# Kernel tuning notes

Hardware: AMD Instinct MI355X
Metric: run time of the kernel (lower is better)

Reference implementation:

```python
import jax, jax.numpy as jnp
import numpy as np

MODEL_DIM = 4096
HEAD_DIM = 128
N_HEADS = 32
N_KV_HEADS = 8
B = 2
S = 2048
ROPE_BASE = 10000.0


def _rope(v, pos):
    """Interleaved-pair rotary embedding (Llama style). v: [b, s, h, d]."""
    d = v.shape[-1]
    half = d // 2
    inv_freq = 1.0 / (ROPE_BASE ** (jnp.arange(half, dtype=jnp.float32) * 2.0 / d))
    t = pos + jnp.arange(v.shape[1], dtype=jnp.float32)          # [s]
    ang = t[:, None] * inv_freq                                   # [s, half]
    cos = jnp.cos(ang)[None, :, None, :].astype(v.dtype)          # [1, s, 1, half]
    sin = jnp.sin(ang)[None, :, None, :].astype(v.dtype)
    x1 = v[..., 0::2]
    x2 = v[..., 1::2]
    o1 = x1 * cos - x2 * sin
    o2 = x1 * sin + x2 * cos
    return jnp.stack([o1, o2], axis=-1).reshape(v.shape)


def setup_inputs() -> dict:
    key = jax.random.key(0)
    kx, kq, kk, kv, ko = jax.random.split(key, 5)
    wscale = MODEL_DIM ** -0.5  # keep pre-softmax logits in a sane range
    x = jax.random.normal(kx, (B, S, MODEL_DIM), dtype=jnp.float32)
    wq = jax.random.normal(kq, (HEAD_DIM * N_HEADS, MODEL_DIM), dtype=jnp.float32) * wscale
    wk = jax.random.normal(kk, (HEAD_DIM * N_KV_HEADS, MODEL_DIM), dtype=jnp.float32) * wscale
    wv = jax.random.normal(kv, (HEAD_DIM * N_KV_HEADS, MODEL_DIM), dtype=jnp.float32) * wscale
    wo = jax.random.normal(ko, (HEAD_DIM * N_HEADS, MODEL_DIM), dtype=jnp.float32).T * wscale
    wo = jnp.asarray(wo)  # [MODEL_DIM, HEAD_DIM*N_HEADS] like nn.Linear weight
    # causal additive mask, as SDPA attn_mask (float): 0 on/below diag, -inf above
    causal = jnp.tril(jnp.ones((S, S), dtype=bool))
    mask = jnp.where(causal, 0.0, -jnp.inf).astype(jnp.float32)
    return {"x": x, "wq": wq, "wk": wk, "wv": wv, "wo": wo, "mask": mask, "pos": 0}


def reference(x, wq, wk, wv, wo, mask, pos):
    b, s, _ = x.shape
    rep = N_HEADS // N_KV_HEADS
    q = (x @ wq.T).reshape(b, s, N_HEADS, HEAD_DIM)
    k = (x @ wk.T).reshape(b, s, N_KV_HEADS, HEAD_DIM)
    v = (x @ wv.T).reshape(b, s, N_KV_HEADS, HEAD_DIM)
    q = _rope(q, pos)
    k = _rope(k, pos)
    # With pos=0 prefill, the kv-cache slice [:, :pos+s] equals k, v just written.
    # GQA without materializing repeat_interleave: group q heads by kv head.
    qg = q.reshape(b, s, N_KV_HEADS, rep, HEAD_DIM)
    scale = HEAD_DIM ** -0.5
    scores = jnp.einsum('bqhrd,bkhd->bhrqk', qg, k) * scale        # [b, kvh, rep, s, s]
    scores = scores + mask                                          # broadcast [s, s]
    p = jax.nn.softmax(scores, axis=-1)
    out = jnp.einsum('bhrqk,bkhd->bqhrd', p, v).reshape(b, s, N_HEADS * HEAD_DIM)
    return out @ wo.T
```

## Files before the change

### kernel.cpp

```cpp
#include <hip/hip_runtime.h>
#include <hip/hip_bf16.h>
#include <stdint.h>

#define MODEL_DIM 4096
#define HEAD_DIM  128
#define NH        32
#define NKV       8
#define BB        2
#define SS        2048
#define ROWS      (BB*SS)
#define QKVN      (MODEL_DIM + 2*NKV*HEAD_DIM)
#define KOFF      MODEL_DIM
#define VOFF      (MODEL_DIM + NKV*HEAD_DIM)
#define SCALE_QK  0.08838834764831845f

typedef __attribute__((ext_vector_type(8))) short short8;
typedef __attribute__((ext_vector_type(4))) float f32x4;

static __device__ __forceinline__ unsigned short f2bf(float f) {
  union { float f; unsigned u; } v; v.f = f;
  unsigned r = v.u + 0x7fffu + ((v.u >> 16) & 1u);
  return (unsigned short)(r >> 16);
}
static __device__ __forceinline__ float bf2f(unsigned short u) {
  union { unsigned u; float f; } v; v.u = ((unsigned)u) << 16;
  return v.f;
}

__global__ void cvt_bf16(const float* __restrict__ s, unsigned short* __restrict__ d, int n4) {
  int i = blockIdx.x * blockDim.x + threadIdx.x;
  int st = gridDim.x * blockDim.x;
  for (; i < n4; i += st) {
    float4 v = reinterpret_cast<const float4*>(s)[i];
    ushort4 o;
    o.x = f2bf(v.x); o.y = f2bf(v.y); o.z = f2bf(v.z); o.w = f2bf(v.w);
    reinterpret_cast<ushort4*>(d)[i] = o;
  }
}

template<int OUT_F32>
__global__ __launch_bounds__(256) void gemm_bt(
    const unsigned short* __restrict__ A, const unsigned short* __restrict__ B,
    void* __restrict__ Cv, int M, int N, int K)
{
  __shared__ unsigned short As[128 * 32];
  __shared__ unsigned short Bs[128 * 32];
  const int tid  = threadIdx.x;
  const int lane = tid & 63;
  const int w    = tid >> 6;

  const int nwg = gridDim.x;
  const int bid = blockIdx.x;
  const int q8  = nwg >> 3;
  const int wg  = (bid & 7) * q8 + (bid >> 3);
  const int gm  = M >> 7;
  const int bm  = wg % gm, bn = wg / gm;
  const int m0  = bm << 7, n0 = bn << 7;
  const int wm  = (w >> 1) << 6, wn = (w & 1) << 6;

  f32x4 acc[4][4] = {};

  const int rowA = lane >> 2;
  const int ch8  = (lane & 3) * 8;

  for (int k0 = 0; k0 < K; k0 += 32) {
    __syncthreads();
    #pragma unroll
    for (int i = 0; i < 2; ++i) {
      const unsigned short* ga = A + (size_t)(m0 + i*64 + w*16 + rowA) * K + k0 + ch8;
      __builtin_amdgcn_global_load_lds((const __attribute__((address_space(1))) void*)ga,
          (__attribute__((address_space(3))) void*)&As[(i*64 + w*16) * 32], 16, 0, 0);
      const unsigned short* gb = B + (size_t)(n0 + i*64 + w*16 + rowA) * K + k0 + ch8;
      __builtin_amdgcn_global_load_lds((const __attribute__((address_space(1))) void*)gb,
          (__attribute__((address_space(3))) void*)&Bs[(i*64 + w*16) * 32], 16, 0, 0);
    }
    __syncthreads();

    short8 af[4], bf[4];
    const int fr = lane & 15, fg = lane >> 4;
    #pragma unroll
    for (int r = 0; r < 4; ++r)
      af[r] = *(const short8*)&As[(wm + r*16 + fr) * 32 + fg * 8];
    #pragma unroll
    for (int r = 0; r < 4; ++r)
      bf[r] = *(const short8*)&Bs[(wn + r*16 + fr) * 32 + fg * 8];
    #pragma unroll
    for (int i = 0; i < 4; ++i)
      #pragma unroll
      for (int j = 0; j < 4; ++j)
        acc[i][j] = __builtin_amdgcn_mfma_f32_16x16x32_bf16(af[i], bf[j], acc[i][j], 0, 0, 0);
  }

  const int cr = (lane >> 4) * 4, cc = lane & 15;
  #pragma unroll
  for (int i = 0; i < 4; ++i)
    #pragma unroll
    for (int j = 0; j < 4; ++j) {
      const int gr = m0 + wm + i*16 + cr;
      const int gc = n0 + wn + j*16 + cc;
      #pragma unroll
      for (int e = 0; e < 4; ++e) {
        const float v = acc[i][j][e];
        if (OUT_F32) ((float*)Cv)[(size_t)(gr + e) * N + gc] = v;
        else ((unsigned short*)Cv)[(size_t)(gr + e) * N + gc] = f2bf(v);
      }
    }
}

__global__ void rope_kernel(unsigned short* __restrict__ qkv, const int* __restrict__ posp) {
  const int row = blockIdx.x;
  const float t = (float)((row & (SS - 1)) + posp[0]);
  const float c0 = -13.28771237954945f / 64.0f;
  for (int i = threadIdx.x; i < (NH + NKV) * 64; i += blockDim.x) {
    const int hh = i >> 6, p = i & 63;
    const int colbase = (hh < NH) ? hh * HEAD_DIM : KOFF + (hh - NH) * HEAD_DIM;
    const float inv = exp2f((float)p * c0);
    float sn, cs;
    sincosf(t * inv, &sn, &cs);
    const size_t base = (size_t)row * QKVN + colbase + 2 * p;
    const float x1 = bf2f(qkv[base]), x2 = bf2f(qkv[base + 1]);
    qkv[base]     = f2bf(x1 * cs - x2 * sn);
    qkv[base + 1] = f2bf(x1 * sn + x2 * cs);
  }
}

#define QBLK 64
#define KVB  64
#define LDK  136
#define LDP  72

static __device__ __forceinline__ int vt_off(int d, int kv) {
  const int byte = (kv << 1) ^ ((((d & 7) ^ ((d >> 3) & 7))) << 4);
  return (d << 6) + (byte >> 1);
}

static __device__ __forceinline__ float bcast_row16(float v0, float v1, float v2, float v3, int lane) {
  const int sel = (lane >> 2) & 3;
  const float a = (sel & 1) ? v1 : v0;
  const float b = (sel & 1) ? v3 : v2;
  const float m = (sel & 2) ? b : a;
  const int q = lane & 15;
  return __shfl(m, ((q >> 2) << 4) + ((q & 3) << 2));
}

__global__ __launch_bounds__(256) void attn_kernel(
    const unsigned short* __restrict__ qkv, unsigned short* __restrict__ out)
{
  __shared__ unsigned short Ks[KVB * LDK];
  __shared__ unsigned short Vt[HEAD_DIM * KVB];
  __shared__ unsigned short Ps[4 * 16 * LDP];

  const int tid  = threadIdx.x;
  const int lane = tid & 63;
  const int w    = tid >> 6;
  const int bh   = blockIdx.y;
  const int b    = bh >> 5, h = bh & 31;
  const int kvh  = h >> 2;
  const int q0   = (gridDim.x - 1 - blockIdx.x) * QBLK;
  const int fr   = lane & 15, fg = lane >> 4;

  const size_t qrow0 = (size_t)(b * SS + q0 + w * 16);
  short8 qf[4];
  #pragma unroll
  for (int kk = 0; kk < 4; ++kk)
    qf[kk] = *(const short8*)&qkv[(qrow0 + fr) * QKVN + h * HEAD_DIM + kk * 32 + fg * 8];

  f32x4 ot[8] = {};
  float m_run[4], l_run[4];
  #pragma unroll
  for (int i = 0; i < 4; ++i) { m_run[i] = -INFINITY; l_run[i] = 0.f; }

  const int ntile = (q0 >> 6) + 1;
  for (int jt = 0; jt < ntile; ++jt) {
    const int j0 = jt * KVB;
    const bool diag = (jt == ntile - 1);
    __syncthreads();
    #pragma unroll
    for (int it = 0; it < 4; ++it) {
      const int cid = it * 256 + tid;
      const int row = cid >> 4, c8 = (cid & 15) << 3;
      const size_t grow = (size_t)(b * SS + j0 + row);
      *(uint4*)&Ks[row * LDK + c8] = *(const uint4*)&qkv[grow * QKVN + KOFF + kvh * HEAD_DIM + c8];
      uint4 vv = *(const uint4*)&qkv[grow * QKVN + VOFF + kvh * HEAD_DIM + c8];
      const unsigned short* v8 = (const unsigned short*)&vv;
      #pragma unroll
      for (int e = 0; e < 8; ++e)
        Vt[vt_off(c8 + e, row)] = v8[e];
    }
    __syncthreads();

    float pv[4][4];
    #pragma unroll
    for (int ct = 0; ct < 4; ++ct) {
      f32x4 s = {};
      #pragma unroll
      for (int kk = 0; kk < 4; ++kk) {
        const short8 kf = *(const short8*)&Ks[(ct * 16 + fr) * LDK + kk * 32 + fg * 8];
        s = __builtin_amdgcn_mfma_f32_16x16x32_bf16(qf[kk], kf, s, 0, 0, 0);
      }
      #pragma unroll
      for (int i = 0; i < 4; ++i) {
        float v = s[i] * SCALE_QK;
        if (diag) {
          const int qr = w * 16 + fg * 4 + i;
          const int kc = ct * 16 + fr;
          if (kc > qr) v = -INFINITY;
        }
        pv[ct][i] = v;
      }
    }

    float resc[4];
    #pragma unroll
    for (int i = 0; i < 4; ++i) {
      float mx = fmaxf(fmaxf(pv[0][i], pv[1][i]), fmaxf(pv[2][i], pv[3][i]));
      #pragma unroll
      for (int d = 1; d < 16; d <<= 1) mx = fmaxf(mx, __shfl_xor(mx, d));
      const float nm = fmaxf(m_run[i], mx);
      resc[i] = expf(m_run[i] - nm);
      m_run[i] = nm;
      float sum = 0.f;
      #pragma unroll
      for (int ct = 0; ct < 4; ++ct) {
        const float e = expf(pv[ct][i] - nm);
        pv[ct][i] = e;
        sum += e;
      }
      #pragma unroll
      for (int d = 1; d < 16; d <<= 1) sum += __shfl_xor(sum, d);
      l_run[i] = l_run[i] * resc[i] + sum;
    }

    unsigned short* Pw = &Ps[w * 16 * LDP];
    #pragma unroll
    for (int ct = 0; ct < 4; ++ct)
      #pragma unroll
      for (int i = 0; i < 4; ++i)
        Pw[(fg * 4 + i) * LDP + ct * 16 + fr] = f2bf(pv[ct][i]);

    const float rq = bcast_row16(resc[0], resc[1], resc[2], resc[3], lane);
    #pragma unroll
    for (int oc = 0; oc < 8; ++oc)
      #pragma unroll
      for (int e = 0; e < 4; ++e) ot[oc][e] *= rq;

    #pragma unroll
    for (int kk2 = 0; kk2 < 2; ++kk2) {
      const short8 pf = *(const short8*)&Pw[fr * LDP + kk2 * 32 + fg * 8];
      #pragma unroll
      for (int oc = 0; oc < 8; ++oc) {
        const short8 vf = *(const short8*)&Vt[vt_off(oc * 16 + fr, kk2 * 32 + fg * 8)];
        ot[oc] = __builtin_amdgcn_mfma_f32_16x16x32_bf16(vf, pf, ot[oc], 0, 0, 0);
      }
    }
  }

  const float invq = bcast_row16(1.f / l_run[0], 1.f / l_run[1],
                                 1.f / l_run[2], 1.f / l_run[3], lane);
  const size_t orow = (size_t)(b * SS + q0 + w * 16) + (lane & 15);
  #pragma unroll
  for (int oc = 0; oc < 8; ++oc) {
    const unsigned short e0 = f2bf(ot[oc][0] * invq);
    const unsigned short e1 = f2bf(ot[oc][1] * invq);
    const unsigned short e2 = f2bf(ot[oc][2] * invq);
    const unsigned short e3 = f2bf(ot[oc][3] * invq);
    const uint2 val = make_uint2((unsigned)e0 | ((unsigned)e1 << 16),
                                 (unsigned)e2 | ((unsigned)e3 << 16));
    *(uint2*)&out[orow * MODEL_DIM + h * HEAD_DIM + oc * 16 + fg * 4] = val;
  }
}

extern "C" void kernel_launch(void* const* d_in, const int* in_sizes, int n_in,
                              void* d_out, int out_size, void* d_ws, size_t ws_size,
                              hipStream_t stream) {
  const float* x  = (const float*)d_in[0];
  const float* wq = (const float*)d_in[1];
  const float* wk = (const float*)d_in[2];
  const float* wv = (const float*)d_in[3];
  const float* wo = (const float*)d_in[4];
  const int* pos  = (const int*)d_in[6];
  float* out = (float*)d_out;

  unsigned short* xb   = (unsigned short*)d_ws;
  unsigned short* wqkv = xb   + (size_t)ROWS * MODEL_DIM;
  unsigned short* wob  = wqkv + (size_t)QKVN * MODEL_DIM;
  unsigned short* qkv  = wob  + (size_t)MODEL_DIM * MODEL_DIM;
  unsigned short* attn = qkv  + (size_t)ROWS * QKVN;

  cvt_bf16<<<2048, 256, 0, stream>>>(x,  xb,   ROWS * MODEL_DIM / 4);
  cvt_bf16<<<2048, 256, 0, stream>>>(wq, wqkv, MODEL_DIM * MODEL_DIM / 4);
  cvt_bf16<<<1024, 256, 0, stream>>>(wk, wqkv + (size_t)MODEL_DIM * MODEL_DIM,          NKV * HEAD_DIM * MODEL_DIM / 4);
  cvt_bf16<<<1024, 256, 0, stream>>>(wv, wqkv + (size_t)(MODEL_DIM + NKV * HEAD_DIM) * MODEL_DIM, NKV * HEAD_DIM * MODEL_DIM / 4);
  cvt_bf16<<<2048, 256, 0, stream>>>(wo, wob,  MODEL_DIM * MODEL_DIM / 4);

  gemm_bt<0><<<dim3((ROWS / 128) * (QKVN / 128)), 256, 0, stream>>>(xb, wqkv, qkv, ROWS, QKVN, MODEL_DIM);
  rope_kernel<<<ROWS, 256, 0, stream>>>(qkv, pos);
  attn_kernel<<<dim3(SS / QBLK, BB * NH), 256, 0, stream>>>(qkv, attn);
  gemm_bt<1><<<dim3((ROWS / 128) * (MODEL_DIM / 128)), 256, 0, stream>>>(attn, wob, out, ROWS, MODEL_DIM, MODEL_DIM);
}
```

Before: 1.157 ms.

## Pre-transpose V globally and double-buffer K/V tiles via async LDS loads

Adds a separate kernel that transposes V into a [b,kvh,d,s] buffer, reusing the no-longer-needed bf16 x workspace. The attention kernel then fetches K and V^T tiles with direct global-to-LDS loads into double-buffered, XOR-swizzled shared memory, prefetching the next tile while computing the current one. This removes the per-tile scalar transpose scatter into LDS and one barrier per tile, in exchange for an extra kernel launch, extra global traffic for V, and doubled LDS use that may lower occupancy.

After: 1.106 ms. 1.05x faster.

```diff
diff --git a/kernel.cpp b/kernel.cpp
--- a/kernel.cpp
+++ b/kernel.cpp
@@ -26,6 +26,10 @@
   union { unsigned u; float f; } v; v.u = ((unsigned)u) << 16;
   return v.f;
 }
+static __device__ __forceinline__ void glds16(const unsigned short* g, const unsigned short* l) {
+  __builtin_amdgcn_global_load_lds((const __attribute__((address_space(1))) void*)g,
+      (__attribute__((address_space(3))) void*)l, 16, 0, 0);
+}
 
 __global__ void cvt_bf16(const float* __restrict__ s, unsigned short* __restrict__ d, int n4) {
   int i = blockIdx.x * blockDim.x + threadIdx.x;
@@ -68,11 +72,9 @@
     #pragma unroll
     for (int i = 0; i < 2; ++i) {
       const unsigned short* ga = A + (size_t)(m0 + i*64 + w*16 + rowA) * K + k0 + ch8;
-      __builtin_amdgcn_global_load_lds((const __attribute__((address_space(1))) void*)ga,
-          (__attribute__((address_space(3))) void*)&As[(i*64 + w*16) * 32], 16, 0, 0);
+      glds16(ga, &As[(i*64 + w*16) * 32]);
       const unsigned short* gb = B + (size_t)(n0 + i*64 + w*16 + rowA) * K + k0 + ch8;
-      __builtin_amdgcn_global_load_lds((const __attribute__((address_space(1))) void*)gb,
-          (__attribute__((address_space(3))) void*)&Bs[(i*64 + w*16) * 32], 16, 0, 0);
+      glds16(gb, &Bs[(i*64 + w*16) * 32]);
     }
     __syncthreads();
 
@@ -124,15 +126,43 @@
   }
 }
 
+__global__ __launch_bounds__(256) void vtrans_kernel(
+    const unsigned short* __restrict__ qkv, unsigned short* __restrict__ vt)
+{
+  __shared__ unsigned short T[64 * 128];
+  const int tid = threadIdx.x;
+  const int bk  = blockIdx.y;
+  const int s0  = blockIdx.x * 64;
+  const int b   = bk >> 3, kvh = bk & 7;
+
+  #pragma unroll
+  for (int it = 0; it < 4; ++it) {
+    const int cid  = it * 256 + tid;
+    const int s    = cid >> 4, slot = cid & 15;
+    const int sl   = (slot & 8) | ((slot ^ (s >> 3)) & 7);
+    *(uint4*)&T[s * 128 + sl * 8] =
+      *(const uint4*)&qkv[(size_t)(b * SS + s0 + s) * QKVN + VOFF + kvh * HEAD_DIM + slot * 8];
+  }
+  __syncthreads();
+  #pragma unroll
+  for (int it = 0; it < 4; ++it) {
+    const int cid = it * 256 + tid;
+    const int d   = cid >> 3, s8 = (cid & 7) * 8;
+    unsigned short tmp[8];
+    #pragma unroll
+    for (int j = 0; j < 8; ++j) {
+      const int s    = s8 + j;
+      const int slot = d >> 3;
+      const int sl   = (slot & 8) | ((slot ^ (s >> 3)) & 7);
+      tmp[j] = T[s * 128 + sl * 8 + (d & 7)];
+    }
+    *(uint4*)&vt[((size_t)bk * HEAD_DIM + d) * SS + s0 + s8] = *(uint4*)tmp;
+  }
+}
+
 #define QBLK 64
 #define KVB  64
-#define LDK  136
 #define LDP  72
-
-static __device__ __forceinline__ int vt_off(int d, int kv) {
-  const int byte = (kv << 1) ^ ((((d & 7) ^ ((d >> 3) & 7))) << 4);
-  return (d << 6) + (byte >> 1);
-}
 
 static __device__ __forceinline__ float bcast_row16(float v0, float v1, float v2, float v3, int lane) {
   const int sel = (lane >> 2) & 3;
@@ -144,10 +174,11 @@
 }
 
 __global__ __launch_bounds__(256) void attn_kernel(
-    const unsigned short* __restrict__ qkv, unsigned short* __restrict__ out)
+    const unsigned short* __restrict__ qkv, const unsigned short* __restrict__ vt,
+    unsigned short* __restrict__ out)
 {
-  __shared__ unsigned short Ks[KVB * LDK];
-  __shared__ unsigned short Vt[HEAD_DIM * KVB];
+  __shared__ unsigned short Kb[2][KVB * HEAD_DIM];
+  __shared__ unsigned short Vb[2][HEAD_DIM * KVB];
   __shared__ unsigned short Ps[4 * 16 * LDP];
 
   const int tid  = threadIdx.x;
@@ -159,6 +190,9 @@
   const int q0   = (gridDim.x - 1 - blockIdx.x) * QBLK;
   const int fr   = lane & 15, fg = lane >> 4;
 
+  const unsigned short* kg  = qkv + KOFF + kvh * HEAD_DIM;
+  const unsigned short* vtg = vt + (size_t)(b * NKV + kvh) * HEAD_DIM * SS;
+
   const size_t qrow0 = (size_t)(b * SS + q0 + w * 16);
   short8 qf[4];
   #pragma unroll
@@ -170,32 +204,55 @@
   #pragma unroll
   for (int i = 0; i < 4; ++i) { m_run[i] = -INFINITY; l_run[i] = 0.f; }
 
+  const int krow_l = lane >> 4;
+  const int kslot  = lane & 15;
+  const int vrow_l = lane >> 3;
+  const int vslot  = lane & 7;
+
   const int ntile = (q0 >> 6) + 1;
+
+  {
+    const int j0 = 0;
+    #pragma unroll
+    for (int i = 0; i < 4; ++i) {
+      const int r  = w * 16 + i * 4 + krow_l;
+      const int gs = (kslot & 8) | ((kslot ^ r) & 7);
+      glds16(kg + (size_t)(b * SS + j0 + r) * QKVN + gs * 8, &Kb[0][(w * 16 + i * 4) * 128]);
+      const int d  = w * 32 + i * 8 + vrow_l;
+      const int vg = vslot ^ (d & 7);
+      glds16(vtg + (size_t)d * SS + j0 + vg * 8, &Vb[0][(w * 32 + i * 8) * 64]);
+    }
+  }
+
+  int cur = 0;
   for (int jt = 0; jt < ntile; ++jt) {
-    const int j0 = jt * KVB;
+    __syncthreads();
+    if (jt + 1 < ntile) {
+      const int j0n = (jt + 1) * KVB;
+      #pragma unroll
+      for (int i = 0; i < 4; ++i) {
+        const int r  = w * 16 + i * 4 + krow_l;
+        const int gs = (kslot & 8) | ((kslot ^ r) & 7);
+        glds16(kg + (size_t)(b * SS + j0n + r) * QKVN + gs * 8, &Kb[cur ^ 1][(w * 16 + i * 4) * 128]);
+        const int d  = w * 32 + i * 8 + vrow_l;
+        const int vg = vslot ^ (d & 7);
+        glds16(vtg + (size_t)d * SS + j0n + vg * 8, &Vb[cur ^ 1][(w * 32 + i * 8) * 64]);
+      }
+    }
+    const unsigned short* Kc = Kb[cur];
+    const unsigned short* Vc = Vb[cur];
     const bool diag = (jt == ntile - 1);
-    __syncthreads();
-    #pragma unroll
-    for (int it = 0; it < 4; ++it) {
-      const int cid = it * 256 + tid;
-      const int row = cid >> 4, c8 = (cid & 15) << 3;
-      const size_t grow = (size_t)(b * SS + j0 + row);
-      *(uint4*)&Ks[row * LDK + c8] = *(const uint4*)&qkv[grow * QKVN + KOFF + kvh * HEAD_DIM + c8];
-      uint4 vv = *(const uint4*)&qkv[grow * QKVN + VOFF + kvh * HEAD_DIM + c8];
-      const unsigned short* v8 = (const unsigned short*)&vv;
-      #pragma unroll
-      for (int e = 0; e < 8; ++e)
-        Vt[vt_off(c8 + e, row)] = v8[e];
-    }
-    __syncthreads();
 
     float pv[4][4];
     #pragma unroll
     for (int ct = 0; ct < 4; ++ct) {
       f32x4 s = {};
+      const int krow = ct * 16 + fr;
       #pragma unroll
       for (int kk = 0; kk < 4; ++kk) {
-        const short8 kf = *(const short8*)&Ks[(ct * 16 + fr) * LDK + kk * 32 + fg * 8];
+        const int c  = kk * 4 + fg;
+        const int sl = (c & 8) | ((c ^ krow) & 7);
+        const short8 kf = *(const short8*)&Kc[krow * 128 + sl * 8];
         s = __builtin_amdgcn_mfma_f32_16x16x32_bf16(qf[kk], kf, s, 0, 0, 0);
       }
       #pragma unroll
@@ -249,10 +306,13 @@
       const short8 pf = *(const short8*)&Pw[fr * LDP + kk2 * 32 + fg * 8];
       #pragma unroll
       for (int oc = 0; oc < 8; ++oc) {
-        const short8 vf = *(const short8*)&Vt[vt_off(oc * 16 + fr, kk2 * 32 + fg * 8)];
+        const int vd = oc * 16 + fr;
+        const int sl = (kk2 * 4 + fg) ^ (vd & 7);
+        const short8 vf = *(const short8*)&Vc[vd * 64 + sl * 8];
         ot[oc] = __builtin_amdgcn_mfma_f32_16x16x32_bf16(vf, pf, ot[oc], 0, 0, 0);
       }
     }
+    cur ^= 1;
   }
 
   const float invq = bcast_row16(1.f / l_run[0], 1.f / l_run[1],
@@ -286,6 +346,7 @@
   unsigned short* wob  = wqkv + (size_t)QKVN * MODEL_DIM;
   unsigned short* qkv  = wob  + (size_t)MODEL_DIM * MODEL_DIM;
   unsigned short* attn = qkv  + (size_t)ROWS * QKVN;
+  unsigned short* vtb  = xb;
 
   cvt_bf16<<<2048, 256, 0, stream>>>(x,  xb,   ROWS * MODEL_DIM / 4);
   cvt_bf16<<<2048, 256, 0, stream>>>(wq, wqkv, MODEL_DIM * MODEL_DIM / 4);
@@ -295,6 +356,7 @@
 
   gemm_bt<0><<<dim3((ROWS / 128) * (QKVN / 128)), 256, 0, stream>>>(xb, wqkv, qkv, ROWS, QKVN, MODEL_DIM);
   rope_kernel<<<ROWS, 256, 0, stream>>>(qkv, pos);
-  attn_kernel<<<dim3(SS / QBLK, BB * NH), 256, 0, stream>>>(qkv, attn);
+  vtrans_kernel<<<dim3(SS / 64, BB * NKV), 256, 0, stream>>>(qkv, vtb);
+  attn_kernel<<<dim3(SS / QBLK, BB * NH), 256, 0, stream>>>(qkv, vtb, attn);
   gemm_bt<1><<<dim3((ROWS / 128) * (MODEL_DIM / 128)), 256, 0, stream>>>(attn, wob, out, ROWS, MODEL_DIM, MODEL_DIM);
 }
```
